# Kernel tuning notes

Hardware: AMD Instinct MI355X
Metric: run time of the kernel (lower is better)

Reference implementation:

```python
import jax, jax.numpy as jnp
import numpy as np

EPS = 1e-6
N_HEADS = 16


def _stable_softmax(x):
    # max subtracted with stop_gradient (torch .detach()), clamp to [-50, 50], eps in denom
    x_max = jax.lax.stop_gradient(jnp.max(x, axis=-1, keepdims=True))
    exp_x = jnp.exp(jnp.clip(x - x_max, -50.0, 50.0))
    return exp_x / (jnp.sum(exp_x, axis=-1, keepdims=True) + EPS)


def setup_inputs() -> dict:
    key = jax.random.key(0)
    k1, k2, k3 = jax.random.split(key, 3)
    B, S, D = 2, 2048, 1024
    x = jax.random.normal(k1, (B, S, D), dtype=jnp.float32)
    Wqkv = jax.random.normal(k2, (3 * D, D), dtype=jnp.float32) * 0.02
    Wout = jax.random.normal(k3, (D, D), dtype=jnp.float32) * (0.02 / np.sqrt(2))
    return {"x": x, "Wqkv": Wqkv, "Wout": Wout}


def reference(x, Wqkv, Wout):
    B, S, D = x.shape
    H = N_HEADS
    Dh = D // H
    scale = 1.0 / np.sqrt(Dh)
    # qkv projection (torch Linear: x @ W.T), split into q,k,v -> (B,H,S,Dh)
    qkv = (x @ Wqkv.T).reshape(B, S, 3, H, Dh)
    qkv = jnp.transpose(qkv, (2, 0, 3, 1, 4))
    q, k, v = qkv[0], qkv[1], qkv[2]
    # chunked attention is mathematically identical to full attention here
    scores = jnp.einsum('bhqd,bhkd->bhqk', q, k) * scale
    attn = _stable_softmax(scores)
    out = jnp.einsum('bhqk,bhkd->bhqd', attn, v)  # (B,H,S,Dh)
    out = jnp.transpose(out, (0, 2, 1, 3)).reshape(B, S, D)
    return out @ Wout.T
```

## Files before the change

### kernel.cpp

```cpp
#include <hip/hip_runtime.h>
#include <hip/hip_bf16.h>
#include <stdint.h>

#define S_LEN   2048
#define D_MODEL 1024
#define NH      16
#define DH      64
#define BATCH   2
#define TOKENS  (BATCH * S_LEN)

typedef __bf16 bf16;
typedef __bf16 bf16x8 __attribute__((ext_vector_type(8)));
typedef __bf16 b16x4  __attribute__((ext_vector_type(4)));
typedef float  f32x4  __attribute__((ext_vector_type(4)));
typedef float  f32x16 __attribute__((ext_vector_type(16)));
typedef unsigned int uint32;

__device__ __forceinline__ void async_lds16(const void* g, void* l) {
  __builtin_amdgcn_global_load_lds((__attribute__((address_space(1))) void*)g,
                                   (__attribute__((address_space(3))) void*)l,
                                   16, 0, 0);
}

__global__ __launch_bounds__(256) void convert_kernel(
    const float* __restrict__ src, bf16* __restrict__ dst, int n8) {
  const int i = blockIdx.x * 256 + threadIdx.x;
  if (i >= n8) return;
  const f32x4 a = *(const f32x4*)(src + (size_t)i * 8);
  const f32x4 b = *(const f32x4*)(src + (size_t)i * 8 + 4);
  bf16x8 o;
#pragma unroll
  for (int j = 0; j < 4; j++) { o[j] = (bf16)a[j]; o[j + 4] = (bf16)b[j]; }
  *(bf16x8*)(dst + (size_t)i * 8) = o;
}

#define BM 128
#define BN 128
#define BK 32

#define GEMM_CORE(APTR, BPTR, KDIM)                                              \
  __shared__ __align__(16) bf16 As[BM * BK];                                     \
  __shared__ __align__(16) bf16 Bs[BN * BK];                                     \
  const int tid  = threadIdx.x;                                                  \
  const int wave = tid >> 6, lane = tid & 63;                                    \
  const int quad = lane >> 4, l16 = lane & 15;                                   \
  const int m0 = blockIdx.y * BM;                                                \
  const int n0 = blockIdx.x * BN;                                                \
  const int wm = (wave >> 1) * 64, wn = (wave & 1) * 64;                         \
  f32x4 acc[4][4] = {};                                                          \
  const int c0 = tid, c1 = tid + 256;                                            \
  for (int k0 = 0; k0 < (KDIM); k0 += BK) {                                      \
    async_lds16((APTR) + (size_t)(m0 + (c0 >> 2)) * (KDIM) + k0 + (c0 & 3) * 8,  \
                As + c0 * 8);                                                    \
    async_lds16((APTR) + (size_t)(m0 + (c1 >> 2)) * (KDIM) + k0 + (c1 & 3) * 8,  \
                As + c1 * 8);                                                    \
    async_lds16((BPTR) + (size_t)(n0 + (c0 >> 2)) * (KDIM) + k0 + (c0 & 3) * 8,  \
                Bs + c0 * 8);                                                    \
    async_lds16((BPTR) + (size_t)(n0 + (c1 >> 2)) * (KDIM) + k0 + (c1 & 3) * 8,  \
                Bs + c1 * 8);                                                    \
    __syncthreads();                                                             \
    bf16x8 af[4], bfr[4];                                                        \
    _Pragma("unroll") for (int i = 0; i < 4; i++)                                \
        af[i] = *(const bf16x8*)(As + (wm + i * 16 + l16) * BK + quad * 8);      \
    _Pragma("unroll") for (int j = 0; j < 4; j++)                                \
        bfr[j] = *(const bf16x8*)(Bs + (wn + j * 16 + l16) * BK + quad * 8);     \
    _Pragma("unroll") for (int i = 0; i < 4; i++)                                \
      _Pragma("unroll") for (int j = 0; j < 4; j++)                              \
        acc[i][j] = __builtin_amdgcn_mfma_f32_16x16x32_bf16(af[i], bfr[j],       \
                                                            acc[i][j], 0, 0, 0); \
    __syncthreads();                                                             \
  }

__global__ __launch_bounds__(256) void gemm_qkv_kernel(
    const bf16* __restrict__ X, const bf16* __restrict__ W,
    bf16* __restrict__ Qo, bf16* __restrict__ Ko, bf16* __restrict__ VTo) {
  GEMM_CORE(X, W, D_MODEL)
  const int t = n0 >> 10;
#pragma unroll
  for (int i = 0; i < 4; i++) {
    const int rowb = m0 + wm + i * 16 + quad * 4;
    const int b = rowb >> 11, s0 = rowb & 2047;
#pragma unroll
    for (int j = 0; j < 4; j++) {
      const int col = n0 + wn + j * 16 + l16;
      const int h = (col >> 6) & 15, d = col & 63;
      if (t == 2) {
        b16x4 v4;
#pragma unroll
        for (int r = 0; r < 4; r++) v4[r] = (bf16)acc[i][j][r];
        *(b16x4*)(VTo + ((size_t)(b * NH + h) * DH + d) * S_LEN + s0) = v4;
      } else {
#pragma unroll
        for (int r = 0; r < 4; r++) {
          const float v = acc[i][j][r];
          if (t == 0)
            Qo[((size_t)(b * NH + h) * S_LEN + s0 + r) * DH + d] = (bf16)(v * 0.125f);
          else
            Ko[((size_t)(b * NH + h) * S_LEN + s0 + r) * DH + d] = (bf16)v;
        }
      }
    }
  }
}

__global__ __launch_bounds__(256) void gemm_out_kernel(
    const bf16* __restrict__ A, const bf16* __restrict__ W,
    float* __restrict__ Out) {
  GEMM_CORE(A, W, D_MODEL)
#pragma unroll
  for (int i = 0; i < 4; i++) {
    const int rowb = m0 + wm + i * 16 + quad * 4;
#pragma unroll
    for (int j = 0; j < 4; j++) {
      const int col = n0 + wn + j * 16 + l16;
#pragma unroll
      for (int r = 0; r < 4; r++)
        Out[(size_t)(rowb + r) * D_MODEL + col] = acc[i][j][r];
    }
  }
}

__global__ __launch_bounds__(512, 2) void attn_kernel(
    const bf16* __restrict__ Q, const bf16* __restrict__ K,
    const bf16* __restrict__ VT, bf16* __restrict__ AO) {
  __shared__ __align__(16) bf16 smem[2][2][2 * 64 * 64];

  const int tid  = threadIdx.x;
  const int lane = tid & 63;
  const int wave = tid >> 6;
  const int g    = wave >> 2;
  const int qw   = wave & 3;
  const int l31  = lane & 31;
  const int hi   = lane >> 5;
  const int sw   = l31 & 7;

  const int bid = (blockIdx.x & 7) * 32 + (blockIdx.x >> 3);
  const int qb  = bid & 7;
  const int bh  = bid >> 3;

  const bf16* qp = Q  + ((size_t)bh * S_LEN + qb * 256 + qw * 64 + l31) * DH;
  const bf16* kp = K  + (size_t)bh * S_LEN * DH;
  const bf16* vp = VT + (size_t)bh * DH * S_LEN;

  bf16x8 qf0[4], qf1[4];
#pragma unroll
  for (int dk = 0; dk < 4; dk++) {
    qf0[dk] = *(const bf16x8*)(qp + dk * 16 + hi * 8);
    qf1[dk] = *(const bf16x8*)(qp + 32 * DH + dk * 16 + hi * 8);
  }

  const int gtid = tid & 255;
  const int cid0 = gtid, cid1 = gtid + 256;
  const int r0 = cid0 >> 3, c0 = (cid0 & 7) ^ (r0 & 7);
  const int r1 = cid1 >> 3, c1 = (cid1 & 7) ^ (r1 & 7);
  const bf16* ka0 = kp + (size_t)(g * 64 + r0) * DH + c0 * 8;
  const bf16* ka1 = kp + (size_t)(g * 64 + r1) * DH + c1 * 8;
  const bf16* va0 = vp + (size_t)r0 * S_LEN + g * 64 + c0 * 8;
  const bf16* va1 = vp + (size_t)r1 * S_LEN + g * 64 + c1 * 8;
  const int ld0 = cid0 * 8, ld1 = cid1 * 8;

  f32x16 oT0[2] = {}, oT1[2] = {};
  float lsum0 = 0.f, lsum1 = 0.f;

  bf16* sg = &smem[g][0][0];

#define STAGE(B)                                                                 \
  {                                                                              \
    bf16* s = sg + (B) * (2 * 64 * 64);                                          \
    async_lds16(ka0, s + ld0);                                                   \
    async_lds16(ka1, s + ld1);                                                   \
    async_lds16(va0, s + 4096 + ld0);                                            \
    async_lds16(va1, s + 4096 + ld1);                                            \
    ka0 += 8192; ka1 += 8192; va0 += 128; va1 += 128;                            \
  }

  STAGE(0)

  for (int t = 0; t < 16; t++) {
    const int cur = t & 1;
    if (t < 15) {
      STAGE(cur ^ 1)
      asm volatile("s_waitcnt vmcnt(4)" ::: "memory");
    } else {
      asm volatile("s_waitcnt vmcnt(0)" ::: "memory");
    }
    __builtin_amdgcn_s_barrier();
    __builtin_amdgcn_s_setprio(1);

    const bf16* sb = sg + cur * (2 * 64 * 64);

    f32x16 st0[2] = {}, st1[2] = {};
#pragma unroll
    for (int kt = 0; kt < 2; kt++)
#pragma unroll
      for (int dk = 0; dk < 4; dk++) {
        const bf16x8 kf = *(const bf16x8*)(sb + (kt * 32 + l31) * 64 +
                                           (((dk * 2 + hi) ^ sw) * 8));
        st0[kt] = __builtin_amdgcn_mfma_f32_32x32x16_bf16(kf, qf0[dk], st0[kt], 0, 0, 0);
        st1[kt] = __builtin_amdgcn_mfma_f32_32x32x16_bf16(kf, qf1[dk], st1[kt], 0, 0, 0);
      }

#pragma unroll
    for (int kt = 0; kt < 2; kt++)
#pragma unroll
      for (int hk = 0; hk < 2; hk++) {
        const int ks = kt * 2 + hk;
        float e0[8], e1[8];
#pragma unroll
        for (int r = 0; r < 8; r++) e0[r] = __expf(st0[kt][hk * 8 + r]);
#pragma unroll
        for (int r = 0; r < 8; r++) e1[r] = __expf(st1[kt][hk * 8 + r]);
        lsum0 += ((e0[0] + e0[1]) + (e0[2] + e0[3])) + ((e0[4] + e0[5]) + (e0[6] + e0[7]));
        lsum1 += ((e1[0] + e1[1]) + (e1[2] + e1[3])) + ((e1[4] + e1[5]) + (e1[6] + e1[7]));
        uint32 p00, p01, p02, p03, p10, p11, p12, p13;
        asm("v_cvt_pk_bf16_f32 %0, %1, %2" : "=v"(p00) : "v"(e0[0]), "v"(e0[1]));
        asm("v_cvt_pk_bf16_f32 %0, %1, %2" : "=v"(p01) : "v"(e0[2]), "v"(e0[3]));
        asm("v_cvt_pk_bf16_f32 %0, %1, %2" : "=v"(p02) : "v"(e0[4]), "v"(e0[5]));
        asm("v_cvt_pk_bf16_f32 %0, %1, %2" : "=v"(p03) : "v"(e0[6]), "v"(e0[7]));
        asm("v_cvt_pk_bf16_f32 %0, %1, %2" : "=v"(p10) : "v"(e1[0]), "v"(e1[1]));
        asm("v_cvt_pk_bf16_f32 %0, %1, %2" : "=v"(p11) : "v"(e1[2]), "v"(e1[3]));
        asm("v_cvt_pk_bf16_f32 %0, %1, %2" : "=v"(p12) : "v"(e1[4]), "v"(e1[5]));
        asm("v_cvt_pk_bf16_f32 %0, %1, %2" : "=v"(p13) : "v"(e1[6]), "v"(e1[7]));
        asm("v_permlane32_swap_b32 %0, %1" : "+v"(p00), "+v"(p02));
        asm("v_permlane32_swap_b32 %0, %1" : "+v"(p01), "+v"(p03));
        asm("v_permlane32_swap_b32 %0, %1" : "+v"(p10), "+v"(p12));
        asm("v_permlane32_swap_b32 %0, %1" : "+v"(p11), "+v"(p13));
        union { uint32 u[4]; bf16x8 v; } pf0, pf1;
        pf0.u[0] = p00; pf0.u[1] = p01; pf0.u[2] = p02; pf0.u[3] = p03;
        pf1.u[0] = p10; pf1.u[1] = p11; pf1.u[2] = p12; pf1.u[3] = p13;
#pragma unroll
        for (int dt = 0; dt < 2; dt++) {
          const bf16x8 vf = *(const bf16x8*)(sb + 4096 + (dt * 32 + l31) * 64 +
                                             (((ks * 2 + hi) ^ sw) * 8));
          oT0[dt] = __builtin_amdgcn_mfma_f32_32x32x16_bf16(vf, pf0.v, oT0[dt], 0, 0, 0);
          oT1[dt] = __builtin_amdgcn_mfma_f32_32x32x16_bf16(vf, pf1.v, oT1[dt], 0, 0, 0);
        }
      }

    __builtin_amdgcn_s_setprio(0);
    asm volatile("s_waitcnt lgkmcnt(0)" ::: "memory");
    __builtin_amdgcn_s_barrier();
  }
#undef STAGE

  lsum0 += __shfl_xor(lsum0, 32);
  lsum1 += __shfl_xor(lsum1, 32);

  float* mO = (float*)&smem[0][0][0];
  float* mL = mO + 256 * 32;
  const int mrow = qw * 64 + lane;

  if (g == 1) {
#pragma unroll
    for (int j = 0; j < 8; j++) {
      const int dt = j >> 2, rb = (j & 3) * 4;
      f32x4 c = { oT0[dt][rb], oT0[dt][rb + 1], oT0[dt][rb + 2], oT0[dt][rb + 3] };
      *(f32x4*)((char*)mO + mrow * 128 + ((j ^ (lane & 7)) * 16)) = c;
    }
    mL[mrow] = lsum0;
  }
  __syncthreads();
  if (g == 0) {
#pragma unroll
    for (int j = 0; j < 8; j++) {
      const int dt = j >> 2, rb = (j & 3) * 4;
      const f32x4 c = *(const f32x4*)((char*)mO + mrow * 128 + ((j ^ (lane & 7)) * 16));
#pragma unroll
      for (int rr = 0; rr < 4; rr++) oT0[dt][rb + rr] += c[rr];
    }
    lsum0 += mL[mrow];
  }
  __syncthreads();
  if (g == 1) {
#pragma unroll
    for (int j = 0; j < 8; j++) {
      const int dt = j >> 2, rb = (j & 3) * 4;
      f32x4 c = { oT1[dt][rb], oT1[dt][rb + 1], oT1[dt][rb + 2], oT1[dt][rb + 3] };
      *(f32x4*)((char*)mO + mrow * 128 + ((j ^ (lane & 7)) * 16)) = c;
    }
    mL[mrow] = lsum1;
  }
  __syncthreads();
  if (g == 0) {
#pragma unroll
    for (int j = 0; j < 8; j++) {
      const int dt = j >> 2, rb = (j & 3) * 4;
      const f32x4 c = *(const f32x4*)((char*)mO + mrow * 128 + ((j ^ (lane & 7)) * 16));
#pragma unroll
      for (int rr = 0; rr < 4; rr++) oT1[dt][rb + rr] += c[rr];
    }
    lsum1 += mL[mrow];

    const float inv0 = 1.0f / (lsum0 + 1e-6f);
    const float inv1 = 1.0f / (lsum1 + 1e-6f);
    const int b = bh >> 4, h = bh & 15;
    const int srow = qb * 256 + qw * 64 + l31;
    const size_t base0 = (size_t)(b * S_LEN + srow) * D_MODEL + h * DH;
    const size_t base1 = base0 + (size_t)32 * D_MODEL;
#pragma unroll
    for (int dt = 0; dt < 2; dt++)
#pragma unroll
      for (int rg = 0; rg < 4; rg++) {
        b16x4 o4;
#pragma unroll
        for (int rr = 0; rr < 4; rr++) o4[rr] = (bf16)(oT0[dt][rg * 4 + rr] * inv0);
        *(b16x4*)(AO + base0 + dt * 32 + rg * 8 + hi * 4) = o4;
      }
#pragma unroll
    for (int dt = 0; dt < 2; dt++)
#pragma unroll
      for (int rg = 0; rg < 4; rg++) {
        b16x4 o4;
#pragma unroll
        for (int rr = 0; rr < 4; rr++) o4[rr] = (bf16)(oT1[dt][rg * 4 + rr] * inv1);
        *(b16x4*)(AO + base1 + dt * 32 + rg * 8 + hi * 4) = o4;
      }
  }
}

extern "C" void kernel_launch(void* const* d_in, const int* in_sizes, int n_in,
                              void* d_out, int out_size, void* d_ws, size_t ws_size,
                              hipStream_t stream) {
  const float* x    = (const float*)d_in[0];
  const float* wqkv = (const float*)d_in[1];
  const float* wout = (const float*)d_in[2];
  float* out = (float*)d_out;

  bf16* Q  = (bf16*)d_ws;
  bf16* K  = Q  + (size_t)TOKENS * D_MODEL;
  bf16* VT = K  + (size_t)TOKENS * D_MODEL;
  bf16* xb = VT + (size_t)TOKENS * D_MODEL;
  bf16* AO = xb;
  bf16* wqkvb = (bf16*)d_out;
  bf16* woutb = Q;

  convert_kernel<<<dim3(TOKENS * D_MODEL / (256 * 8)), dim3(256), 0, stream>>>(
      x, xb, TOKENS * D_MODEL / 8);
  convert_kernel<<<dim3(3 * D_MODEL * D_MODEL / (256 * 8)), dim3(256), 0, stream>>>(
      wqkv, wqkvb, 3 * D_MODEL * D_MODEL / 8);

  gemm_qkv_kernel<<<dim3(3 * D_MODEL / BN, TOKENS / BM), dim3(256), 0, stream>>>(
      xb, wqkvb, Q, K, VT);

  attn_kernel<<<dim3(BATCH * NH * (S_LEN / 256)), dim3(512), 0, stream>>>(Q, K, VT, AO);

  convert_kernel<<<dim3(D_MODEL * D_MODEL / (256 * 8)), dim3(256), 0, stream>>>(
      wout, woutb, D_MODEL * D_MODEL / 8);

  gemm_out_kernel<<<dim3(D_MODEL / BN, TOKENS / BM), dim3(256), 0, stream>>>(
      AO, woutb, out);
}
```

Measured before the change: 186.6 us.

## Load K/V fragments directly from global into registers, drop LDS staging

The attention loop no longer stages K and V tiles through shared memory with async global-to-LDS copies and barriers. Each lane now loads its MFMA operand fragments straight from global memory into registers, with the next K tile register-double-buffered and V loaded at the start of each step. This removes the per-iteration barriers and LDS traffic, at the cost of redundant global/L2 reads across the four query waves that share a tile, higher register pressure, and exposed load latency for V.

```diff
diff --git a/kernel.cpp b/kernel.cpp
--- a/kernel.cpp
+++ b/kernel.cpp
@@ -120,10 +120,83 @@
   }
 }
 
+__device__ __forceinline__ void attn_body(
+    const bf16* __restrict__ klane, const bf16* __restrict__ vlane, int t,
+    const bf16x8 (&KU)[8], bf16x8 (&KP)[8], bf16x8 (&vf)[8],
+    const bf16x8 (&qf0)[4], const bf16x8 (&qf1)[4],
+    f32x16 (&oT0)[2], f32x16 (&oT1)[2], float& lsum0, float& lsum1) {
+#pragma unroll
+  for (int dt = 0; dt < 2; dt++)
+#pragma unroll
+    for (int ks = 0; ks < 4; ks++)
+      vf[dt * 4 + ks] =
+          *(const bf16x8*)(vlane + dt * (32 * S_LEN) + t * 128 + ks * 16);
+  if (t < 15) {
+#pragma unroll
+    for (int kt = 0; kt < 2; kt++)
+#pragma unroll
+      for (int dk = 0; dk < 4; dk++)
+        KP[kt * 4 + dk] =
+            *(const bf16x8*)(klane + (t + 1) * 8192 + kt * 2048 + dk * 16);
+  }
+
+  f32x16 st0[2] = {}, st1[2] = {};
+  __builtin_amdgcn_s_setprio(1);
+#pragma unroll
+  for (int kt = 0; kt < 2; kt++)
+#pragma unroll
+    for (int dk = 0; dk < 4; dk++) {
+      st0[kt] = __builtin_amdgcn_mfma_f32_32x32x16_bf16(KU[kt * 4 + dk], qf0[dk],
+                                                        st0[kt], 0, 0, 0);
+      st1[kt] = __builtin_amdgcn_mfma_f32_32x32x16_bf16(KU[kt * 4 + dk], qf1[dk],
+                                                        st1[kt], 0, 0, 0);
+    }
+  __builtin_amdgcn_s_setprio(0);
+
+#pragma unroll
+  for (int kt = 0; kt < 2; kt++)
+#pragma unroll
+    for (int hk = 0; hk < 2; hk++) {
+      const int ks = kt * 2 + hk;
+      float e0[8], e1[8];
+#pragma unroll
+      for (int r = 0; r < 8; r++) e0[r] = __expf(st0[kt][hk * 8 + r]);
+#pragma unroll
+      for (int r = 0; r < 8; r++) e1[r] = __expf(st1[kt][hk * 8 + r]);
+      lsum0 += ((e0[0] + e0[1]) + (e0[2] + e0[3])) + ((e0[4] + e0[5]) + (e0[6] + e0[7]));
+      lsum1 += ((e1[0] + e1[1]) + (e1[2] + e1[3])) + ((e1[4] + e1[5]) + (e1[6] + e1[7]));
+      uint32 p00, p01, p02, p03, p10, p11, p12, p13;
+      asm("v_cvt_pk_bf16_f32 %0, %1, %2" : "=v"(p00) : "v"(e0[0]), "v"(e0[1]));
+      asm("v_cvt_pk_bf16_f32 %0, %1, %2" : "=v"(p01) : "v"(e0[2]), "v"(e0[3]));
+      asm("v_cvt_pk_bf16_f32 %0, %1, %2" : "=v"(p02) : "v"(e0[4]), "v"(e0[5]));
+      asm("v_cvt_pk_bf16_f32 %0, %1, %2" : "=v"(p03) : "v"(e0[6]), "v"(e0[7]));
+      asm("v_cvt_pk_bf16_f32 %0, %1, %2" : "=v"(p10) : "v"(e1[0]), "v"(e1[1]));
+      asm("v_cvt_pk_bf16_f32 %0, %1, %2" : "=v"(p11) : "v"(e1[2]), "v"(e1[3]));
+      asm("v_cvt_pk_bf16_f32 %0, %1, %2" : "=v"(p12) : "v"(e1[4]), "v"(e1[5]));
+      asm("v_cvt_pk_bf16_f32 %0, %1, %2" : "=v"(p13) : "v"(e1[6]), "v"(e1[7]));
+      asm("v_permlane32_swap_b32 %0, %1" : "+v"(p00), "+v"(p02));
+      asm("v_permlane32_swap_b32 %0, %1" : "+v"(p01), "+v"(p03));
+      asm("v_permlane32_swap_b32 %0, %1" : "+v"(p10), "+v"(p12));
+      asm("v_permlane32_swap_b32 %0, %1" : "+v"(p11), "+v"(p13));
+      union { uint32 u[4]; bf16x8 v; } pf0, pf1;
+      pf0.u[0] = p00; pf0.u[1] = p01; pf0.u[2] = p02; pf0.u[3] = p03;
+      pf1.u[0] = p10; pf1.u[1] = p11; pf1.u[2] = p12; pf1.u[3] = p13;
+      __builtin_amdgcn_s_setprio(1);
+#pragma unroll
+      for (int dt = 0; dt < 2; dt++) {
+        oT0[dt] = __builtin_amdgcn_mfma_f32_32x32x16_bf16(vf[dt * 4 + ks], pf0.v,
+                                                          oT0[dt], 0, 0, 0);
+        oT1[dt] = __builtin_amdgcn_mfma_f32_32x32x16_bf16(vf[dt * 4 + ks], pf1.v,
+                                                          oT1[dt], 0, 0, 0);
+      }
+      __builtin_amdgcn_s_setprio(0);
+    }
+}
+
 __global__ __launch_bounds__(512, 2) void attn_kernel(
     const bf16* __restrict__ Q, const bf16* __restrict__ K,
     const bf16* __restrict__ VT, bf16* __restrict__ AO) {
-  __shared__ __align__(16) bf16 smem[2][2][2 * 64 * 64];
+  __shared__ __align__(16) float msm[256 * 32 + 256];
 
   const int tid  = threadIdx.x;
   const int lane = tid & 63;
@@ -132,15 +205,14 @@
   const int qw   = wave & 3;
   const int l31  = lane & 31;
   const int hi   = lane >> 5;
-  const int sw   = l31 & 7;
 
   const int bid = (blockIdx.x & 7) * 32 + (blockIdx.x >> 3);
   const int qb  = bid & 7;
   const int bh  = bid >> 3;
 
-  const bf16* qp = Q  + ((size_t)bh * S_LEN + qb * 256 + qw * 64 + l31) * DH;
-  const bf16* kp = K  + (size_t)bh * S_LEN * DH;
-  const bf16* vp = VT + (size_t)bh * DH * S_LEN;
+  const bf16* qp = Q + ((size_t)bh * S_LEN + qb * 256 + qw * 64 + l31) * DH;
+  const bf16* klane = K + (size_t)bh * S_LEN * DH + (size_t)(g * 64 + l31) * DH + hi * 8;
+  const bf16* vlane = VT + (size_t)bh * DH * S_LEN + (size_t)l31 * S_LEN + g * 64 + hi * 8;
 
   bf16x8 qf0[4], qf1[4];
 #pragma unroll
@@ -149,105 +221,26 @@
     qf1[dk] = *(const bf16x8*)(qp + 32 * DH + dk * 16 + hi * 8);
   }
 
-  const int gtid = tid & 255;
-  const int cid0 = gtid, cid1 = gtid + 256;
-  const int r0 = cid0 >> 3, c0 = (cid0 & 7) ^ (r0 & 7);
-  const int r1 = cid1 >> 3, c1 = (cid1 & 7) ^ (r1 & 7);
-  const bf16* ka0 = kp + (size_t)(g * 64 + r0) * DH + c0 * 8;
-  const bf16* ka1 = kp + (size_t)(g * 64 + r1) * DH + c1 * 8;
-  const bf16* va0 = vp + (size_t)r0 * S_LEN + g * 64 + c0 * 8;
-  const bf16* va1 = vp + (size_t)r1 * S_LEN + g * 64 + c1 * 8;
-  const int ld0 = cid0 * 8, ld1 = cid1 * 8;
-
   f32x16 oT0[2] = {}, oT1[2] = {};
   float lsum0 = 0.f, lsum1 = 0.f;
 
-  bf16* sg = &smem[g][0][0];
-
-#define STAGE(B)                                                                 \
-  {                                                                              \
-    bf16* s = sg + (B) * (2 * 64 * 64);                                          \
-    async_lds16(ka0, s + ld0);                                                   \
-    async_lds16(ka1, s + ld1);                                                   \
-    async_lds16(va0, s + 4096 + ld0);                                            \
-    async_lds16(va1, s + 4096 + ld1);                                            \
-    ka0 += 8192; ka1 += 8192; va0 += 128; va1 += 128;                            \
-  }
-
-  STAGE(0)
-
-  for (int t = 0; t < 16; t++) {
-    const int cur = t & 1;
-    if (t < 15) {
-      STAGE(cur ^ 1)
-      asm volatile("s_waitcnt vmcnt(4)" ::: "memory");
-    } else {
-      asm volatile("s_waitcnt vmcnt(0)" ::: "memory");
-    }
-    __builtin_amdgcn_s_barrier();
-    __builtin_amdgcn_s_setprio(1);
-
-    const bf16* sb = sg + cur * (2 * 64 * 64);
-
-    f32x16 st0[2] = {}, st1[2] = {};
-#pragma unroll
-    for (int kt = 0; kt < 2; kt++)
-#pragma unroll
-      for (int dk = 0; dk < 4; dk++) {
-        const bf16x8 kf = *(const bf16x8*)(sb + (kt * 32 + l31) * 64 +
-                                           (((dk * 2 + hi) ^ sw) * 8));
-        st0[kt] = __builtin_amdgcn_mfma_f32_32x32x16_bf16(kf, qf0[dk], st0[kt], 0, 0, 0);
-        st1[kt] = __builtin_amdgcn_mfma_f32_32x32x16_bf16(kf, qf1[dk], st1[kt], 0, 0, 0);
-      }
-
-#pragma unroll
-    for (int kt = 0; kt < 2; kt++)
-#pragma unroll
-      for (int hk = 0; hk < 2; hk++) {
-        const int ks = kt * 2 + hk;
-        float e0[8], e1[8];
-#pragma unroll
-        for (int r = 0; r < 8; r++) e0[r] = __expf(st0[kt][hk * 8 + r]);
-#pragma unroll
-        for (int r = 0; r < 8; r++) e1[r] = __expf(st1[kt][hk * 8 + r]);
-        lsum0 += ((e0[0] + e0[1]) + (e0[2] + e0[3])) + ((e0[4] + e0[5]) + (e0[6] + e0[7]));
-        lsum1 += ((e1[0] + e1[1]) + (e1[2] + e1[3])) + ((e1[4] + e1[5]) + (e1[6] + e1[7]));
-        uint32 p00, p01, p02, p03, p10, p11, p12, p13;
-        asm("v_cvt_pk_bf16_f32 %0, %1, %2" : "=v"(p00) : "v"(e0[0]), "v"(e0[1]));
-        asm("v_cvt_pk_bf16_f32 %0, %1, %2" : "=v"(p01) : "v"(e0[2]), "v"(e0[3]));
-        asm("v_cvt_pk_bf16_f32 %0, %1, %2" : "=v"(p02) : "v"(e0[4]), "v"(e0[5]));
-        asm("v_cvt_pk_bf16_f32 %0, %1, %2" : "=v"(p03) : "v"(e0[6]), "v"(e0[7]));
-        asm("v_cvt_pk_bf16_f32 %0, %1, %2" : "=v"(p10) : "v"(e1[0]), "v"(e1[1]));
-        asm("v_cvt_pk_bf16_f32 %0, %1, %2" : "=v"(p11) : "v"(e1[2]), "v"(e1[3]));
-        asm("v_cvt_pk_bf16_f32 %0, %1, %2" : "=v"(p12) : "v"(e1[4]), "v"(e1[5]));
-        asm("v_cvt_pk_bf16_f32 %0, %1, %2" : "=v"(p13) : "v"(e1[6]), "v"(e1[7]));
-        asm("v_permlane32_swap_b32 %0, %1" : "+v"(p00), "+v"(p02));
-        asm("v_permlane32_swap_b32 %0, %1" : "+v"(p01), "+v"(p03));
-        asm("v_permlane32_swap_b32 %0, %1" : "+v"(p10), "+v"(p12));
-        asm("v_permlane32_swap_b32 %0, %1" : "+v"(p11), "+v"(p13));
-        union { uint32 u[4]; bf16x8 v; } pf0, pf1;
-        pf0.u[0] = p00; pf0.u[1] = p01; pf0.u[2] = p02; pf0.u[3] = p03;
-        pf1.u[0] = p10; pf1.u[1] = p11; pf1.u[2] = p12; pf1.u[3] = p13;
-#pragma unroll
-        for (int dt = 0; dt < 2; dt++) {
-          const bf16x8 vf = *(const bf16x8*)(sb + 4096 + (dt * 32 + l31) * 64 +
-                                             (((ks * 2 + hi) ^ sw) * 8));
-          oT0[dt] = __builtin_amdgcn_mfma_f32_32x32x16_bf16(vf, pf0.v, oT0[dt], 0, 0, 0);
-          oT1[dt] = __builtin_amdgcn_mfma_f32_32x32x16_bf16(vf, pf1.v, oT1[dt], 0, 0, 0);
-        }
-      }
-
-    __builtin_amdgcn_s_setprio(0);
-    asm volatile("s_waitcnt lgkmcnt(0)" ::: "memory");
-    __builtin_amdgcn_s_barrier();
-  }
-#undef STAGE
+  bf16x8 kA[8], kB[8], vf[8];
+#pragma unroll
+  for (int kt = 0; kt < 2; kt++)
+#pragma unroll
+    for (int dk = 0; dk < 4; dk++)
+      kA[kt * 4 + dk] = *(const bf16x8*)(klane + kt * 2048 + dk * 16);
+
+  for (int tt = 0; tt < 8; tt++) {
+    attn_body(klane, vlane, 2 * tt,     kA, kB, vf, qf0, qf1, oT0, oT1, lsum0, lsum1);
+    attn_body(klane, vlane, 2 * tt + 1, kB, kA, vf, qf0, qf1, oT0, oT1, lsum0, lsum1);
+  }
 
   lsum0 += __shfl_xor(lsum0, 32);
   lsum1 += __shfl_xor(lsum1, 32);
 
-  float* mO = (float*)&smem[0][0][0];
-  float* mL = mO + 256 * 32;
+  float* mO = msm;
+  float* mL = msm + 256 * 32;
   const int mrow = qw * 64 + lane;
 
   if (g == 1) {
```

After: 239.1 us. 28.1% more time.
